# Kernel tuning notes

Hardware: AMD Instinct MI355X
Metric: run time of the kernel (lower is better)

Reference implementation:

```python
import jax, jax.numpy as jnp
import numpy as np

B, T, P, D, V = 8, 4096, 4, 512, 256
N = T // P          # 1024 patches (T divisible by P, so no padding needed)
K = 16              # k_retrieval
W = 4               # local message-passing window
H = 8               # refresh attention heads = min(8, D//64)
ROUNDS = 6
EPS = 1e-5


def layer_norm(x, g, b):
    mu = x.mean(-1, keepdims=True)
    var = ((x - mu) ** 2).mean(-1, keepdims=True)
    return (x - mu) / jnp.sqrt(var + EPS) * g + b


def setup_inputs() -> dict:
    key = jax.random.key(0)
    ks = iter(jax.random.split(key, 48))
    w = lambda *s: jax.random.normal(next(ks), s, jnp.float32) * 0.02
    p = {}
    p['x'] = jax.random.randint(next(ks), (B, T), 0, V)
    p['emb'] = w(V, D)
    p['pos_emb'] = w(P, D)
    p['gru_w_ih'] = w(D, 3 * D); p['gru_w_hh'] = w(D, 3 * D)
    p['gru_b_ih'] = jnp.zeros(3 * D); p['gru_b_hh'] = jnp.zeros(3 * D)
    p['patch_ln_g'] = jnp.ones(D); p['patch_ln_b'] = jnp.zeros(D)
    p['summ_w'] = w(D, D); p['summ_b'] = jnp.zeros(D)
    p['msg_w1'] = w(2 * D, D); p['msg_b1'] = jnp.zeros(D)
    p['msg_w2'] = w(D, D); p['msg_b2'] = jnp.zeros(D)
    p['msg_ln_g'] = jnp.ones(D); p['msg_ln_b'] = jnp.zeros(D)
    p['q_w'] = w(D, D); p['q_b'] = jnp.zeros(D)
    p['k_w'] = w(D, D); p['k_b'] = jnp.zeros(D)
    p['v_w'] = w(D, D); p['v_b'] = jnp.zeros(D)
    p['o_w'] = w(D, D); p['o_b'] = jnp.zeros(D)
    p['gc_w_ih'] = w(2 * D, 3 * D); p['gc_w_hh'] = w(D, 3 * D)
    p['gc_b_ih'] = jnp.zeros(3 * D); p['gc_b_hh'] = jnp.zeros(3 * D)
    p['ar_ln_g'] = jnp.ones(D); p['ar_ln_b'] = jnp.zeros(D)
    p['ar_qkv_w'] = w(D, 3 * D); p['ar_qkv_b'] = jnp.zeros(3 * D)
    p['ar_out_w'] = w(D, D); p['ar_out_b'] = jnp.zeros(D)
    p['broad_w'] = w(D, D); p['broad_b'] = jnp.zeros(D)
    p['ln_g'] = jnp.ones(D); p['ln_b'] = jnp.zeros(D)
    p['head_w'] = w(D, V)
    return p


def reference(x, emb, pos_emb, gru_w_ih, gru_w_hh, gru_b_ih, gru_b_hh,
              patch_ln_g, patch_ln_b, summ_w, summ_b,
              msg_w1, msg_b1, msg_w2, msg_b2, msg_ln_g, msg_ln_b,
              q_w, q_b, k_w, k_b, v_w, v_b, o_w, o_b,
              gc_w_ih, gc_w_hh, gc_b_ih, gc_b_hh,
              ar_ln_g, ar_ln_b, ar_qkv_w, ar_qkv_b, ar_out_w, ar_out_b,
              broad_w, broad_b, ln_g, ln_b, head_w):
    # --- patch encoding: embedding + pos + GRU over the P tokens of each patch ---
    flat = x.reshape(B * N, P)
    h = emb[flat] + pos_emb[None, :, :]                      # [B*N, P, D]

    def gru_step(hprev, xt):
        gi = xt @ gru_w_ih + gru_b_ih
        gh = hprev @ gru_w_hh + gru_b_hh
        ir, iz, inn = jnp.split(gi, 3, -1)
        hr, hz, hn = jnp.split(gh, 3, -1)
        r = jax.nn.sigmoid(ir + hr)
        z = jax.nn.sigmoid(iz + hz)
        n = jnp.tanh(inn + r * hn)
        hnew = (1 - z) * n + z * hprev
        return hnew, hnew

    _, hs = jax.lax.scan(gru_step, jnp.zeros((B * N, D), h.dtype), jnp.swapaxes(h, 0, 1))
    local = layer_norm(jnp.swapaxes(hs, 0, 1), patch_ln_g, patch_ln_b).reshape(B, N, P, D)
    h = local.mean(2) @ summ_w + summ_b                      # patch summaries [B, N, D]

    # --- RoPE tables over patch positions ---
    d = D // 2
    inv_freq = 1.0 / (10000.0 ** (jnp.arange(0, D, 2, dtype=jnp.float32) / D))
    freqs = jnp.arange(N, dtype=jnp.float32)[:, None] * inv_freq[None, :]   # [N, d]
    cos, sin = jnp.cos(freqs), jnp.sin(freqs)

    def rotary(t):
        t1, t2 = t[..., :d], t[..., d:]
        return jnp.concatenate([t1 * cos - t2 * sin, t2 * cos + t1 * sin], -1)

    causal = jnp.tril(jnp.ones((N, N), bool))
    hd = D // H

    for rnd in range(ROUNDS):
        # windowed neighbor gather (W past patches + self), fused MLP messages
        padded = jnp.pad(h, ((0, 0), (W, 0), (0, 0)))
        neighbors = jnp.stack([padded[:, W - w:W - w + N] for w in range(W + 1)], 2)  # [B,N,W+1,D]
        self_exp = jnp.broadcast_to(h[:, :, None, :], neighbors.shape)
        msg_in = jnp.concatenate([self_exp, neighbors], -1)
        msgs = (jax.nn.gelu(msg_in @ msg_w1 + msg_b1, approximate=False) @ msg_w2 + msg_b2).mean(2)

        # RoPE top-k sparse causal attention (N > K, sparse branch always taken)
        q = rotary(h @ q_w + q_b)
        k = rotary(h @ k_w + k_b)
        v = h @ v_w + v_b
        scores = jnp.einsum('bnd,bmd->bnm', q, k) / jnp.sqrt(jnp.float32(D))
        scores = jnp.where(causal, scores, -jnp.inf)
        tv, ti = jax.lax.top_k(scores, K)
        probs = jax.nn.softmax(tv, -1)  # == softmax of -inf-filled sparse score matrix
        vg = jax.vmap(lambda vi, ii: vi[ii])(v, ti)          # [B, N, K, D]
        retrieved = jnp.einsum('bnk,bnkd->bnd', probs, vg) @ o_w + o_b

        # GRUCell gated write
        wi = jnp.concatenate([msgs, retrieved], -1)
        gi = wi @ gc_w_ih + gc_b_ih
        gh = h @ gc_w_hh + gc_b_hh
        ir, iz, inn = jnp.split(gi, 3, -1)
        hr, hz, hn = jnp.split(gh, 3, -1)
        r = jax.nn.sigmoid(ir + hr)
        z = jax.nn.sigmoid(iz + hz)
        n = jnp.tanh(inn + r * hn)
        h = layer_norm((1 - z) * n + z * h, msg_ln_g, msg_ln_b)

        # global causal MHA refresh every 2 rounds (eval mode, no dropout)
        if (rnd + 1) % 2 == 0:
            res = h
            hn_ = layer_norm(h, ar_ln_g, ar_ln_b)
            qkv = hn_ @ ar_qkv_w + ar_qkv_b
            qh, kh, vh = [t.reshape(B, N, H, hd) for t in jnp.split(qkv, 3, -1)]
            s = jnp.einsum('bnhd,bmhd->bhnm', qh, kh) / jnp.sqrt(jnp.float32(hd))
            a = jax.nn.softmax(jnp.where(causal, s, -jnp.inf), -1)
            o = jnp.einsum('bhnm,bmhd->bnhd', a, vh).reshape(B, N, D)
            h = res + (o @ ar_out_w + ar_out_b)

    # broadcast patch state back to tokens, project to vocab
    broad = h @ broad_w + broad_b
    final = (local + broad[:, :, None, :]).reshape(B, N * P, D)[:, :T]
    return layer_norm(final, ln_g, ln_b) @ head_w            # [B, T, V]
```

## Files before the change

kernel.cpp:

```cpp
#include <hip/hip_runtime.h>
#include <math.h>

constexpr int CB = 8, CT = 4096, CP = 4, CD = 512, CV = 256;
constexpr int CN = 1024, CK = 16, CH = 8, CHD = 64;
constexpr int ROWS = CB * CN;
constexpr int TROWS = CB * CT;
constexpr float CEPS = 1e-5f;
constexpr size_t PN = (size_t)ROWS * CD;

constexpr size_t OFF_LOCAL = 0;
constexpr size_t OFF_HP    = OFF_LOCAL + (size_t)ROWS * CP * CD;
constexpr size_t OFF_X4    = OFF_HP    + PN;
constexpr size_t OFF_MS    = OFF_X4    + (size_t)ROWS * 2560;
constexpr size_t OFF_A     = OFF_MS    + PN;
constexpr size_t OFF_B     = OFF_A     + PN;
constexpr size_t OFF_BIAS  = OFF_B     + PN;
constexpr size_t OFF_WT    = OFF_BIAS  + 4096;

constexpr size_t TOT_W    = 7471104;
constexpr size_t T_GRU_IH = 0;
constexpr size_t T_GRU_HH = 786432;
constexpr size_t T_SUMM   = 1572864;
constexpr size_t T_FUSE   = 1835008;
constexpr size_t T_MSG2   = 3145728;
constexpr size_t T_OW     = 3407872;
constexpr size_t T_GCAB   = 3670016;
constexpr size_t T_GC_HH  = 5242880;
constexpr size_t T_AR_QKV = 6029312;
constexpr size_t T_AR_OUT = 6815744;
constexpr size_t T_BROAD  = 7077888;
constexpr size_t T_HEAD   = 7340032;

constexpr int F_ACC_F32  = 1;
constexpr int F_ACC_PAIR = 2;
constexpr int F_WR_F32   = 4;
constexpr int F_WR_PAIR  = 8;
constexpr int F_TRI      = 16;
constexpr int F_SPLIT    = 32;

typedef __attribute__((ext_vector_type(8))) short short8;
typedef __attribute__((ext_vector_type(4))) float f32x4;

__device__ __forceinline__ float sigm(float x) { return 1.f / (1.f + expf(-x)); }
__device__ __forceinline__ float geluf(float x) {
  return 0.5f * x * (1.f + erff(x * 0.7071067811865475f));
}
__device__ __forceinline__ unsigned short bf_hi(float x) {
  const unsigned u = __float_as_uint(x);
  return (unsigned short)((u + 0x7FFFu + ((u >> 16) & 1u)) >> 16);
}
__device__ __forceinline__ float bf_f(unsigned short h) {
  return __uint_as_float((unsigned)h << 16);
}
__device__ __forceinline__ void split_store(float v, unsigned short* ph, unsigned short* pl) {
  const unsigned short h = bf_hi(v);
  *ph = h; *pl = bf_hi(v - bf_f(h));
}
__device__ __forceinline__ float blk_sum(float v, float* red) {
#pragma unroll
  for (int o = 32; o > 0; o >>= 1) v += __shfl_down(v, o, 64);
  const int wv = threadIdx.x >> 6, ln = threadIdx.x & 63;
  __syncthreads();
  if (ln == 0) red[wv] = v;
  __syncthreads();
  return red[0] + red[1] + red[2] + red[3];
}

typedef __attribute__((address_space(1))) const unsigned int* gp1_t;
typedef __attribute__((address_space(3))) unsigned int* lp3_t;
__device__ __forceinline__ void gll16(const void* g, void* l) {
  __builtin_amdgcn_global_load_lds((gp1_t)g, (lp3_t)l, 16, 0, 0);
}

__device__ __forceinline__ int swz(int row, int quad) {
  return ((row & ~7) << 5) | (quad << 6) | ((row & 7) << 3);
}

__global__ __launch_bounds__(256) void transpose_split(const float* __restrict__ in,
                                                       unsigned short* __restrict__ oh,
                                                       unsigned short* __restrict__ ol,
                                                       int K, int N, int ldk, int ko)
{
  __shared__ float tile[32][33];
  const int n0 = blockIdx.x * 32, k0 = blockIdx.y * 32;
  const int tx = threadIdx.x & 31, ty = threadIdx.x >> 5;
#pragma unroll
  for (int i = 0; i < 32; i += 8)
    tile[ty + i][tx] = in[(size_t)(k0 + ty + i) * N + n0 + tx];
  __syncthreads();
#pragma unroll
  for (int i = 0; i < 32; i += 8) {
    const float v = tile[tx][ty + i];
    const unsigned short h = bf_hi(v);
    const size_t o = (size_t)(n0 + ty + i) * ldk + ko + k0 + tx;
    oh[o] = h;
    ol[o] = bf_hi(v - bf_f(h));
  }
}

__global__ void concat_bias5(const float* __restrict__ b1, const float* __restrict__ qb,
                             const float* __restrict__ kb, const float* __restrict__ vb,
                             float* __restrict__ o)
{
  const int i = blockIdx.x * 256 + threadIdx.x;
  float v;
  if (i < 512) v = b1[i];
  else if (i < 1024) v = 0.f;
  else if (i < 1536) v = qb[i - 1024];
  else if (i < 2048) v = kb[i - 1536];
  else v = vb[i - 2048];
  o[i] = v;
}

template <bool P3>
__global__ __launch_bounds__(256, 2) void gemm_bf3(
    const unsigned short* __restrict__ AH, const unsigned short* __restrict__ AL,
    const unsigned short* __restrict__ A2H, const unsigned short* __restrict__ A2L,
    int K1, int lda,
    const unsigned short* __restrict__ BH, const unsigned short* __restrict__ BL, int ldb,
    const float* __restrict__ bias, float scale,
    float* __restrict__ Cf, int ldc, float* __restrict__ Cf2,
    unsigned short* __restrict__ CHp, unsigned short* __restrict__ CLp, int ldcp,
    int K, int flags, long long sA, long long sB, long long sC)
{
  AH += (size_t)blockIdx.z * sA; AL += (size_t)blockIdx.z * sA;
  BH += (size_t)blockIdx.z * sB; BL += (size_t)blockIdx.z * sB;
  if (Cf) Cf += (size_t)blockIdx.z * sC;
  int bm, bn;
  if (flags & F_TRI) {
    int t = blockIdx.x, i = 0, acc0 = 0;
    while (acc0 + i + 1 <= t) { ++i; acc0 += i; }
    bm = i << 7; bn = (t - acc0) << 7;
  } else {
    bm = blockIdx.y << 7; bn = blockIdx.x << 7;
  }
  __shared__ __align__(16) unsigned short AsH[128 * 32];
  __shared__ __align__(16) unsigned short AsL[128 * 32];
  __shared__ __align__(16) unsigned short BsH[128 * 32];
  __shared__ __align__(16) unsigned short BsL[P3 ? 128 * 32 : 8];
  const int tid = threadIdx.x;
  const int lane = tid & 63, wave = tid >> 6;
  const int wm = (wave & 1) << 6, wn = (wave >> 1) << 6;
  const int r16 = lane & 15, quad = lane >> 4;
  const int lrow = ((lane >> 5) << 3) | (lane & 7);
  const int lcg8 = ((lane >> 3) & 3) << 3;
  const f32x4 zero = {0.f, 0.f, 0.f, 0.f};
  f32x4 acc[4][4];
#pragma unroll
  for (int i = 0; i < 4; ++i)
#pragma unroll
    for (int j = 0; j < 4; ++j) acc[i][j] = zero;

  for (int k0 = 0; k0 < K; k0 += 32) {
    const bool p1 = (k0 < K1);
    const unsigned short* bAH = p1 ? AH : A2H;
    const unsigned short* bAL = p1 ? AL : A2L;
    const int ka = (p1 ? k0 : k0 - K1) + lcg8;
    const int kb = k0 + lcg8;
#pragma unroll
    for (int i = 0; i < 2; ++i) {
      const int chunk = (wave << 1) | i;
      const size_t ra = (size_t)(bm + (chunk << 4) + lrow) * lda + ka;
      const size_t rb = (size_t)(bn + (chunk << 4) + lrow) * ldb + kb;
      gll16(bAH + ra, &AsH[chunk << 9]);
      gll16(bAL + ra, &AsL[chunk << 9]);
      gll16(BH + rb, &BsH[chunk << 9]);
      if (P3) gll16(BL + rb, &BsL[chunk << 9]);
    }
    __syncthreads();
    short8 bh[4], bl[4];
#pragma unroll
    for (int ni = 0; ni < 4; ++ni) {
      bh[ni] = *(const short8*)&BsH[swz(wn + ni * 16 + r16, quad)];
      if (P3) bl[ni] = *(const short8*)&BsL[swz(wn + ni * 16 + r16, quad)];
    }
#pragma unroll
    for (int mi = 0; mi < 4; ++mi) {
      const short8 ah = *(const short8*)&AsH[swz(wm + mi * 16 + r16, quad)];
      const short8 al = *(const short8*)&AsL[swz(wm + mi * 16 + r16, quad)];
#pragma unroll
      for (int ni = 0; ni < 4; ++ni) {
        acc[mi][ni] = __builtin_amdgcn_mfma_f32_16x16x32_bf16(ah, bh[ni], acc[mi][ni], 0, 0, 0);
        acc[mi][ni] = __builtin_amdgcn_mfma_f32_16x16x32_bf16(al, bh[ni], acc[mi][ni], 0, 0, 0);
        if (P3)
          acc[mi][ni] = __builtin_amdgcn_mfma_f32_16x16x32_bf16(ah, bl[ni], acc[mi][ni], 0, 0, 0);
      }
    }
    __syncthreads();
  }
#pragma unroll
  for (int mi = 0; mi < 4; ++mi) {
    const int row0 = bm + wm + mi * 16 + quad * 4;
#pragma unroll
    for (int ni = 0; ni < 4; ++ni) {
      const int col = bn + wn + ni * 16 + r16;
      const float bv = bias ? bias[col] : 0.f;
#pragma unroll
      for (int rg = 0; rg < 4; ++rg) {
        const int row = row0 + rg;
        float o = acc[mi][ni][rg] * scale + bv;
        if (flags & F_SPLIT) {
          if (col < 1024) {
            float* p = Cf + (size_t)row * ldc + col;
            *p = o + *p;
          } else {
            Cf2[(size_t)row * 512 + (col - 1024)] = o;
          }
        } else {
          if (flags & F_ACC_F32) o += Cf[(size_t)row * ldc + col];
          if (flags & F_ACC_PAIR) {
            const size_t ip = (size_t)row * ldcp + col;
            o += bf_f(CHp[ip]) + bf_f(CLp[ip]);
          }
          if (flags & F_WR_F32) Cf[(size_t)row * ldc + col] = o;
          if (flags & F_WR_PAIR) {
            const size_t ip = (size_t)row * ldcp + col;
            split_store(o, &CHp[ip], &CLp[ip]);
          }
        }
      }
    }
  }
}

__global__ __launch_bounds__(256, 3) void gemm_bf3s(
    const unsigned short* __restrict__ AH, const unsigned short* __restrict__ AL, int lda,
    const unsigned short* __restrict__ BH, int ldb,
    const float* __restrict__ bias,
    float* __restrict__ Cf, int ldc,
    unsigned short* __restrict__ CHp, unsigned short* __restrict__ CLp, int ldcp,
    int K, int flags)
{
  const int bm = blockIdx.y << 6, bn = blockIdx.x << 7;
  __shared__ __align__(16) unsigned short AsH[64 * 32];
  __shared__ __align__(16) unsigned short AsL[64 * 32];
  __shared__ __align__(16) unsigned short BsH[128 * 32];
  const int tid = threadIdx.x;
  const int lane = tid & 63, wave = tid >> 6;
  const int wm = (wave & 1) << 5, wn = (wave >> 1) << 6;
  const int r16 = lane & 15, quad = lane >> 4;
  const int lrow = ((lane >> 5) << 3) | (lane & 7);
  const int lcg8 = ((lane >> 3) & 3) << 3;
  const f32x4 zero = {0.f, 0.f, 0.f, 0.f};
  f32x4 acc[2][4];
#pragma unroll
  for (int i = 0; i < 2; ++i)
#pragma unroll
    for (int j = 0; j < 4; ++j) acc[i][j] = zero;

  for (int k0 = 0; k0 < K; k0 += 32) {
    {
      const size_t ra = (size_t)(bm + (wave << 4) + lrow) * lda + k0 + lcg8;
      gll16(AH + ra, &AsH[wave << 9]);
      gll16(AL + ra, &AsL[wave << 9]);
#pragma unroll
      for (int i = 0; i < 2; ++i) {
        const int chunk = (wave << 1) | i;
        const size_t rb = (size_t)(bn + (chunk << 4) + lrow) * ldb + k0 + lcg8;
        gll16(BH + rb, &BsH[chunk << 9]);
      }
    }
    __syncthreads();
    short8 bh[4];
#pragma unroll
    for (int ni = 0; ni < 4; ++ni)
      bh[ni] = *(const short8*)&BsH[swz(wn + ni * 16 + r16, quad)];
#pragma unroll
    for (int mi = 0; mi < 2; ++mi) {
      const short8 ah = *(const short8*)&AsH[swz(wm + mi * 16 + r16, quad)];
      const short8 al = *(const short8*)&AsL[swz(wm + mi * 16 + r16, quad)];
#pragma unroll
      for (int ni = 0; ni < 4; ++ni) {
        acc[mi][ni] = __builtin_amdgcn_mfma_f32_16x16x32_bf16(ah, bh[ni], acc[mi][ni], 0, 0, 0);
        acc[mi][ni] = __builtin_amdgcn_mfma_f32_16x16x32_bf16(al, bh[ni], acc[mi][ni], 0, 0, 0);
      }
    }
    __syncthreads();
  }
#pragma unroll
  for (int mi = 0; mi < 2; ++mi) {
    const int row0 = bm + wm + mi * 16 + quad * 4;
#pragma unroll
    for (int ni = 0; ni < 4; ++ni) {
      const int col = bn + wn + ni * 16 + r16;
      const float bv = bias ? bias[col] : 0.f;
#pragma unroll
      for (int rg = 0; rg < 4; ++rg) {
        const int row = row0 + rg;
        float o = acc[mi][ni][rg] + bv;
        if (flags & F_ACC_PAIR) {
          const size_t ip = (size_t)row * ldcp + col;
          o += bf_f(CHp[ip]) + bf_f(CLp[ip]);
        }
        if (flags & F_WR_F32) Cf[(size_t)row * ldc + col] = o;
        if (flags & F_WR_PAIR) {
          const size_t ip = (size_t)row * ldcp + col;
          split_store(o, &CHp[ip], &CLp[ip]);
        }
      }
    }
  }
}

__global__ void zero_k(float* __restrict__ p) {
  p[(size_t)blockIdx.x * 256 + threadIdx.x] = 0.f;
}

__global__ void embed_p(const int* __restrict__ x, const float* __restrict__ emb,
                        const float* __restrict__ pos,
                        unsigned short* __restrict__ oh, unsigned short* __restrict__ ol, int t)
{
  const int i = blockIdx.x * 256 + threadIdx.x;
  const int r = i >> 9, d = i & 511;
  const int b = r >> 10, n = r & (CN - 1);
  const int tok = x[b * CT + n * CP + t];
  const float v = emb[(size_t)tok * CD + d] + pos[t * CD + d];
  split_store(v, &oh[i], &ol[i]);
}

__global__ void gru_point_p(const float* __restrict__ gi, const float* __restrict__ ghn,
                            unsigned short* __restrict__ hH, unsigned short* __restrict__ hL,
                            float* __restrict__ hs, int t)
{
  const int i = blockIdx.x * 256 + threadIdx.x;
  const int r = i >> 9, d = i & 511;
  const size_t gb = (size_t)r * (3 * CD) + d;
  const float sr_ = gi[gb], sz = gi[gb + CD], inn = gi[gb + 2 * CD];
  const float hn = ghn[i];
  const float hp = bf_f(hH[i]) + bf_f(hL[i]);
  const float rr = sigm(sr_), zz = sigm(sz);
  const float nn = tanhf(inn + rr * hn);
  const float hv = (1.f - zz) * nn + zz * hp;
  split_store(hv, &hH[i], &hL[i]);
  hs[(size_t)r * (CP * CD) + (size_t)t * CD + d] = hv;
}

__global__ __launch_bounds__(256) void ln_rows(const float* __restrict__ in, float* __restrict__ out,
                                               const float* __restrict__ g, const float* __restrict__ b)
{
  const int r = blockIdx.x, t = threadIdx.x;
  __shared__ float red[4];
  const float* ip = in + (size_t)r * CD;
  const float v0 = ip[t], v1 = ip[t + 256];
  const float mu = blk_sum(v0 + v1, red) * (1.f / CD);
  const float d0 = v0 - mu, d1 = v1 - mu;
  const float var = blk_sum(d0 * d0 + d1 * d1, red) * (1.f / CD);
  const float inv = rsqrtf(var + CEPS);
  float* op = out + (size_t)r * CD;
  op[t] = d0 * inv * g[t] + b[t];
  op[t + 256] = d1 * inv * g[t + 256] + b[t + 256];
}

__global__ void mean_pool_p(const float* __restrict__ local,
                            unsigned short* __restrict__ oh, unsigned short* __restrict__ ol)
{
  const int i = blockIdx.x * 256 + threadIdx.x;
  const int r = i >> 9, d = i & 511;
  const float* p = local + (size_t)r * (CP * CD) + d;
  split_store(0.25f * (p[0] + p[CD] + p[2 * CD] + p[3 * CD]), &oh[i], &ol[i]);
}

__global__ void msg_gelu_p(const float* __restrict__ X4,
                           unsigned short* __restrict__ oh, unsigned short* __restrict__ ol)
{
  const int i = blockIdx.x * 256 + threadIdx.x;
  const int r = i >> 9, d = i & 511;
  const int n = r & (CN - 1);
  const float pv = X4[(size_t)r * 2560 + d];
  float acc = 0.f;
#pragma unroll
  for (int w = 0; w <= 4; ++w) {
    const float xv = pv + ((n >= w) ? X4[(size_t)(r - w) * 2560 + 512 + d] : 0.f);
    acc += geluf(xv);
  }
  split_store(acc * 0.2f, &oh[i], &ol[i]);
}

__global__ void rotary2_p(const float* __restrict__ X4,
                          unsigned short* __restrict__ qh, unsigned short* __restrict__ ql,
                          unsigned short* __restrict__ kh, unsigned short* __restrict__ kl)
{
  const int i = blockIdx.x * 256 + threadIdx.x;
  const int r = i >> 8, j = i & 255;
  const int n = r & (CN - 1);
  const float fr = (float)n * expf(-9.210340371976184f * ((float)j * (1.f / 256.f)));
  float s, c;
  sincosf(fr, &s, &c);
  const float* p = X4 + (size_t)r * 2560;
  const size_t o0 = (size_t)r * CD + j, o1 = o0 + 256;
  const float q1 = p[1024 + j], q2 = p[1024 + 256 + j];
  split_store(q1 * c - q2 * s, &qh[o0], &ql[o0]);
  split_store(q2 * c + q1 * s, &qh[o1], &ql[o1]);
  const float k1 = p[1536 + j], k2 = p[1536 + 256 + j];
  split_store(k1 * c - k2 * s, &kh[o0], &kl[o0]);
  split_store(k2 * c + k1 * s, &kh[o1], &kl[o1]);
}

__global__ __launch_bounds__(256) void topk_attn(const float* __restrict__ X4,
                                                 unsigned short* __restrict__ ctxH,
                                                 unsigned short* __restrict__ ctxL)
{
  const int r = blockIdx.x;
  const int b = r >> 10, n = r & (CN - 1);
  const float* row = X4 + (size_t)r * 2560;
  const int tid = threadIdx.x, lane = tid & 63, wave = tid >> 6;
  __shared__ unsigned long long cands[64];
  __shared__ float p16[CK];
  __shared__ int i16[CK];
  unsigned long long key[4];
#pragma unroll
  for (int q = 0; q < 4; ++q) {
    const int m = tid + q * 256;
    const float v = (m <= n) ? row[m] : -INFINITY;
    unsigned u = __float_as_uint(v);
    u = (u & 0x80000000u) ? ~u : (u | 0x80000000u);
    key[q] = ((unsigned long long)u << 32) | (unsigned)(CN - 1 - m);
  }
  unsigned long long mycand = 0ull;
#pragma unroll
  for (int it = 0; it < CK; ++it) {
    unsigned long long best = key[0];
#pragma unroll
    for (int q = 1; q < 4; ++q) best = best > key[q] ? best : key[q];
#pragma unroll
    for (int o = 32; o > 0; o >>= 1) {
      const unsigned long long o2 = __shfl_xor(best, o, 64);
      best = best > o2 ? best : o2;
    }
    if (lane == it) mycand = best;
#pragma unroll
    for (int q = 0; q < 4; ++q)
      if (key[q] == best) key[q] = 0ull;
  }
  if (lane < CK) cands[wave * CK + lane] = mycand;
  __syncthreads();
  if (wave == 0) {
    unsigned long long k2 = cands[lane];
    unsigned long long mine = 0ull;
#pragma unroll
    for (int it = 0; it < CK; ++it) {
      unsigned long long best = k2;
#pragma unroll
      for (int o = 32; o > 0; o >>= 1) {
        const unsigned long long o2 = __shfl_xor(best, o, 64);
        best = best > o2 ? best : o2;
      }
      if (lane == it) mine = best;
      if (k2 == best) k2 = 0ull;
    }
    unsigned u = (unsigned)(mine >> 32);
    u = (u & 0x80000000u) ? (u & 0x7FFFFFFFu) : ~u;
    const float val = __uint_as_float(u);
    const int idx = CN - 1 - (int)(mine & 0xFFFFFFFFu);
    const float mx = __shfl(val, 0, 64);
    float e = 0.f;
    if (lane < CK && val != -INFINITY) e = expf(val - mx);
    float sum = e;
#pragma unroll
    for (int o = 32; o > 0; o >>= 1) sum += __shfl_xor(sum, o, 64);
    if (lane < CK) {
      p16[lane] = e / sum;
      i16[lane] = idx;
    }
  }
  __syncthreads();
  const size_t vb = ((size_t)b << 10);
#pragma unroll
  for (int pass = 0; pass < 2; ++pass) {
    const int d = tid + pass * 256;
    float a = 0.f;
#pragma unroll
    for (int q = 0; q < CK; ++q)
      a += p16[q] * X4[(vb + i16[q]) * 2560 + 2048 + d];
    split_store(a, &ctxH[(size_t)r * CD + d], &ctxL[(size_t)r * CD + d]);
  }
}

__global__ __launch_bounds__(256) void gru_ln_p(const float* __restrict__ gi, const float* __restrict__ ghn,
                                                unsigned short* __restrict__ hH, unsigned short* __restrict__ hL,
                                                const float* __restrict__ g, const float* __restrict__ b,
                                                unsigned short* __restrict__ aH, unsigned short* __restrict__ aL,
                                                const float* __restrict__ g2, const float* __restrict__ b2)
{
  const int r = blockIdx.x, t = threadIdx.x;
  __shared__ float red[4];
  float u[2];
#pragma unroll
  for (int q = 0; q < 2; ++q) {
    const int d = t + q * 256;
    const size_t gb = (size_t)r * (3 * CD) + d;
    const float sr_ = gi[gb], sz = gi[gb + CD], inn = gi[gb + 2 * CD];
    const float hn = ghn[(size_t)r * CD + d];
    const size_t hi = (size_t)r * CD + d;
    const float hp = bf_f(hH[hi]) + bf_f(hL[hi]);
    const float rr = sigm(sr_), zz = sigm(sz);
    const float nn = tanhf(inn + rr * hn);
    u[q] = (1.f - zz) * nn + zz * hp;
  }
  const float mu = blk_sum(u[0] + u[1], red) * (1.f / CD);
  const float d0 = u[0] - mu, d1 = u[1] - mu;
  const float var = blk_sum(d0 * d0 + d1 * d1, red) * (1.f / CD);
  const float inv = rsqrtf(var + CEPS);
  const float h0 = d0 * inv * g[t] + b[t];
  const float h1 = d1 * inv * g[t + 256] + b[t + 256];
  split_store(h0, &hH[(size_t)r * CD + t], &hL[(size_t)r * CD + t]);
  split_store(h1, &hH[(size_t)r * CD + t + 256], &hL[(size_t)r * CD + t + 256]);
  if (aH) {
    const float mu2 = blk_sum(h0 + h1, red) * (1.f / CD);
    const float e0 = h0 - mu2, e1 = h1 - mu2;
    const float var2 = blk_sum(e0 * e0 + e1 * e1, red) * (1.f / CD);
    const float inv2 = rsqrtf(var2 + CEPS);
    split_store(e0 * inv2 * g2[t] + b2[t], &aH[(size_t)r * CD + t], &aL[(size_t)r * CD + t]);
    split_store(e1 * inv2 * g2[t + 256] + b2[t + 256],
                &aH[(size_t)r * CD + t + 256], &aL[(size_t)r * CD + t + 256]);
  }
}

constexpr int FP = 72;
__global__ __launch_bounds__(256, 3) void flash_attn_p(const unsigned short* __restrict__ qkvH,
                                                       const unsigned short* __restrict__ qkvL,
                                                       unsigned short* __restrict__ outH,
                                                       unsigned short* __restrict__ outL)
{
  __shared__ __align__(16) unsigned short Kh[64 * FP], Kl[64 * FP];
  __shared__ __align__(16) unsigned short Vth[64 * FP], Vtl[64 * FP];
  __shared__ __align__(16) unsigned short Pm[64 * FP];
  const int qt = blockIdx.x, head = blockIdx.y, b = blockIdx.z;
  const int tid = threadIdx.x;
  const int lane = tid & 63, wave = tid >> 6;
  const int r16 = lane & 15, quad = lane >> 4;
  const size_t base = (size_t)b * CN * (3 * CD) + head * CHD;

  short8 qh_r[2], ql_r[2];
  {
    const size_t qoff = base + (size_t)(qt * 64 + wave * 16 + r16) * (3 * CD) + quad * 8;
    const unsigned short* qph = qkvH + qoff;
    const unsigned short* qpl = qkvL + qoff;
    qh_r[0] = *(const short8*)qph;  qh_r[1] = *(const short8*)(qph + 32);
    ql_r[0] = *(const short8*)qpl;  ql_r[1] = *(const short8*)(qpl + 32);
  }
  float m_i[4], l_i[4];
  f32x4 O[4];
  const f32x4 zero = {0.f, 0.f, 0.f, 0.f};
#pragma unroll
  for (int r = 0; r < 4; ++r) { m_i[r] = -INFINITY; l_i[r] = 0.f; }
#pragma unroll
  for (int d = 0; d < 4; ++d) O[d] = zero;

  for (int j = 0; j <= qt; ++j) {
    __syncthreads();
    {
      const int r = tid >> 2, c0 = (tid & 3) << 4;
      const unsigned short* kh = qkvH + base + (size_t)(j * 64 + r) * (3 * CD) + CD + c0;
      const unsigned short* kl = qkvL + base + (size_t)(j * 64 + r) * (3 * CD) + CD + c0;
      *(uint4*)&Kh[r * FP + c0]     = *(const uint4*)kh;
      *(uint4*)&Kh[r * FP + c0 + 8] = *(const uint4*)(kh + 8);
      *(uint4*)&Kl[r * FP + c0]     = *(const uint4*)kl;
      *(uint4*)&Kl[r * FP + c0 + 8] = *(const uint4*)(kl + 8);
      const int rp = (tid >> 3) << 1, c0v = (tid & 7) << 3;
      const unsigned short* v0h = qkvH + base + (size_t)(j * 64 + rp) * (3 * CD) + 2 * CD + c0v;
      const unsigned short* v1h = v0h + 3 * CD;
      const unsigned short* v0l = qkvL + base + (size_t)(j * 64 + rp) * (3 * CD) + 2 * CD + c0v;
      const unsigned short* v1l = v0l + 3 * CD;
      unsigned short xh[8], yh[8], xl[8], yl[8];
      *(uint4*)xh = *(const uint4*)v0h; *(uint4*)yh = *(const uint4*)v1h;
      *(uint4*)xl = *(const uint4*)v0l; *(uint4*)yl = *(const uint4*)v1l;
#pragma unroll
      for (int c = 0; c < 8; ++c) {
        const int R = c0v + c;
        const int col = rp ^ ((R >> 3) << 3);
        *(unsigned*)&Vth[R * FP + col] = (unsigned)xh[c] | ((unsigned)yh[c] << 16);
        *(unsigned*)&Vtl[R * FP + col] = (unsigned)xl[c] | ((unsigned)yl[c] << 16);
      }
    }
    __syncthreads();
    f32x4 S[4];
#pragma unroll
    for (int nt = 0; nt < 4; ++nt) S[nt] = zero;
#pragma unroll
    for (int kh2 = 0; kh2 < 2; ++kh2) {
      const short8 qh = qh_r[kh2];
      const short8 ql = ql_r[kh2];
#pragma unroll
      for (int nt = 0; nt < 4; ++nt) {
        const short8 kkh = *(const short8*)&Kh[(nt * 16 + r16) * FP + kh2 * 32 + quad * 8];
        const short8 kkl = *(const short8*)&Kl[(nt * 16 + r16) * FP + kh2 * 32 + quad * 8];
        S[nt] = __builtin_amdgcn_mfma_f32_16x16x32_bf16(qh, kkh, S[nt], 0, 0, 0);
        S[nt] = __builtin_amdgcn_mfma_f32_16x16x32_bf16(qh, kkl, S[nt], 0, 0, 0);
        S[nt] = __builtin_amdgcn_mfma_f32_16x16x32_bf16(ql, kkh, S[nt], 0, 0, 0);
      }
    }
#pragma unroll
    for (int r = 0; r < 4; ++r) {
      const int qrow = wave * 16 + quad * 4 + r;
      float s[4];
#pragma unroll
      for (int nt = 0; nt < 4; ++nt) {
        s[nt] = S[nt][r] * 0.125f;
        if (j == qt && (nt * 16 + r16) > qrow) s[nt] = -1e30f;
      }
      float rm = fmaxf(fmaxf(s[0], s[1]), fmaxf(s[2], s[3]));
#pragma unroll
      for (int o = 8; o > 0; o >>= 1) rm = fmaxf(rm, __shfl_xor(rm, o, 64));
      const float newm = fmaxf(m_i[r], rm);
      float p[4], rs = 0.f;
#pragma unroll
      for (int nt = 0; nt < 4; ++nt) { p[nt] = expf(s[nt] - newm); rs += p[nt]; }
#pragma unroll
      for (int o = 8; o > 0; o >>= 1) rs += __shfl_xor(rs, o, 64);
      const float alpha = expf(m_i[r] - newm);
      l_i[r] = l_i[r] * alpha + rs;
      m_i[r] = newm;
#pragma unroll
      for (int dt = 0; dt < 4; ++dt) O[dt][r] *= alpha;
#pragma unroll
      for (int nt = 0; nt < 4; ++nt)
        Pm[qrow * FP + nt * 16 + r16] = bf_hi(p[nt]);
    }
    __syncthreads();
#pragma unroll
    for (int kh2 = 0; kh2 < 2; ++kh2) {
      const short8 pa = *(const short8*)&Pm[(wave * 16 + r16) * FP + kh2 * 32 + quad * 8];
#pragma unroll
      for (int dt = 0; dt < 4; ++dt) {
        const int R = dt * 16 + r16;
        const int col = (kh2 * 32 + quad * 8) ^ ((R >> 3) << 3);
        const short8 vh = *(const short8*)&Vth[R * FP + col];
        const short8 vl = *(const short8*)&Vtl[R * FP + col];
        O[dt] = __builtin_amdgcn_mfma_f32_16x16x32_bf16(pa, vh, O[dt], 0, 0, 0);
        O[dt] = __builtin_amdgcn_mfma_f32_16x16x32_bf16(pa, vl, O[dt], 0, 0, 0);
      }
    }
  }
#pragma unroll
  for (int r = 0; r < 4; ++r) {
    const float inv = 1.f / l_i[r];
    const size_t row = (size_t)b * CN + qt * 64 + wave * 16 + quad * 4 + r;
#pragma unroll
    for (int dt = 0; dt < 4; ++dt) {
      const size_t o = row * CD + head * CHD + dt * 16 + r16;
      split_store(O[dt][r] * inv, &outH[o], &outL[o]);
    }
  }
}

__global__ __launch_bounds__(256) void final_ln_p(const float* __restrict__ local,
                                                  const float* __restrict__ broad,
                                                  const float* __restrict__ g, const float* __restrict__ bb,
                                                  unsigned short* __restrict__ oh,
                                                  unsigned short* __restrict__ ol)
{
  const int r = blockIdx.x, t = threadIdx.x;
  __shared__ float red[4];
  const size_t lb = (size_t)r * CD;
  const size_t br = (size_t)(r >> 2) * CD;
  const float v0 = local[lb + t] + broad[br + t];
  const float v1 = local[lb + 256 + t] + broad[br + 256 + t];
  const float mu = blk_sum(v0 + v1, red) * (1.f / CD);
  const float d0 = v0 - mu, d1 = v1 - mu;
  const float var = blk_sum(d0 * d0 + d1 * d1, red) * (1.f / CD);
  const float inv = rsqrtf(var + CEPS);
  split_store(d0 * inv * g[t] + bb[t], &oh[lb + t], &ol[lb + t]);
  split_store(d1 * inv * g[t + 256] + bb[t + 256], &oh[lb + 256 + t], &ol[lb + 256 + t]);
}

extern "C" void kernel_launch(void* const* d_in, const int* in_sizes, int n_in,
                              void* d_out, int out_size, void* d_ws, size_t ws_size,
                              hipStream_t stream)
{
  (void)in_sizes; (void)n_in; (void)out_size; (void)ws_size;
  const int*   x         = (const int*)d_in[0];
  const float* emb       = (const float*)d_in[1];
  const float* pos_emb   = (const float*)d_in[2];
  const float* gru_w_ih  = (const float*)d_in[3];
  const float* gru_w_hh  = (const float*)d_in[4];
  const float* gru_b_ih  = (const float*)d_in[5];
  const float* gru_b_hh  = (const float*)d_in[6];
  const float* patch_g   = (const float*)d_in[7];
  const float* patch_b   = (const float*)d_in[8];
  const float* summ_w    = (const float*)d_in[9];
  const float* summ_b    = (const float*)d_in[10];
  const float* msg_w1    = (const float*)d_in[11];
  const float* msg_b1    = (const float*)d_in[12];
  const float* msg_w2    = (const float*)d_in[13];
  const float* msg_b2    = (const float*)d_in[14];
  const float* msg_ln_g  = (const float*)d_in[15];
  const float* msg_ln_b  = (const float*)d_in[16];
  const float* q_w       = (const float*)d_in[17];
  const float* q_b       = (const float*)d_in[18];
  const float* k_w       = (const float*)d_in[19];
  const float* k_b       = (const float*)d_in[20];
  const float* v_w       = (const float*)d_in[21];
  const float* v_b       = (const float*)d_in[22];
  const float* o_w       = (const float*)d_in[23];
  const float* o_b       = (const float*)d_in[24];
  const float* gc_w_ih   = (const float*)d_in[25];
  const float* gc_w_hh   = (const float*)d_in[26];
  const float* gc_b_ih   = (const float*)d_in[27];
  const float* gc_b_hh   = (const float*)d_in[28];
  const float* ar_ln_g   = (const float*)d_in[29];
  const float* ar_ln_b   = (const float*)d_in[30];
  const float* ar_qkv_w  = (const float*)d_in[31];
  const float* ar_qkv_b  = (const float*)d_in[32];
  const float* ar_out_w  = (const float*)d_in[33];
  const float* ar_out_b  = (const float*)d_in[34];
  const float* broad_w   = (const float*)d_in[35];
  const float* broad_b   = (const float*)d_in[36];
  const float* ln_g      = (const float*)d_in[37];
  const float* ln_b      = (const float*)d_in[38];
  const float* head_w    = (const float*)d_in[39];
  float* out = (float*)d_out;

  float* ws = (float*)d_ws;
  float* WL    = ws + OFF_LOCAL;
  float* X4    = ws + OFF_X4;
  float* GI    = X4;
  float* GHN   = X4 + (size_t)ROWS * 1536;
  float* WBR   = ws + OFF_MS;
  float* Wbias5 = ws + OFF_BIAS;
  unsigned short* WTh = (unsigned short*)(ws + OFF_WT);
  unsigned short* WTl = WTh + TOT_W;
  unsigned short* WhH = (unsigned short*)(ws + OFF_HP);
  unsigned short* WhL = WhH + PN;
  unsigned short* MsH = (unsigned short*)(ws + OFF_MS);
  unsigned short* MsL = MsH + PN;
  unsigned short* pAH = (unsigned short*)(ws + OFF_A);
  unsigned short* pAL = pAH + PN;
  unsigned short* pBH = (unsigned short*)(ws + OFF_B);
  unsigned short* pBL = pBH + PN;
  unsigned short* QkH = (unsigned short*)X4;
  unsigned short* QkL = QkH + (size_t)ROWS * 1536;
  unsigned short* FnH = (unsigned short*)X4;
  unsigned short* FnL = FnH + (size_t)TROWS * CD;

  const int EW = ROWS * CD / 256;
  const float inv_sqrt_d = 0.04419417382415922f;

  auto TR = [&](const float* in, size_t off, int K, int N, int ldk, int ko) {
    transpose_split<<<dim3(N / 32, K / 32), 256, 0, stream>>>(in, WTh + off, WTl + off, K, N, ldk, ko);
  };
  TR(gru_w_ih, T_GRU_IH, 512, 1536, 512, 0);
  TR(gru_w_hh, T_GRU_HH, 512, 1536, 512, 0);
  TR(summ_w,   T_SUMM,   512, 512,  512, 0);
  TR(msg_w1,                      T_FUSE,           512, 512, 512, 0);
  TR(msg_w1 + (size_t)512 * 512,  T_FUSE + 262144,  512, 512, 512, 0);
  TR(q_w,                         T_FUSE + 524288,  512, 512, 512, 0);
  TR(k_w,                         T_FUSE + 786432,  512, 512, 512, 0);
  TR(v_w,                         T_FUSE + 1048576, 512, 512, 512, 0);
  TR(msg_w2,   T_MSG2,   512, 512,  512, 0);
  TR(o_w, T_OW, 512, 512, 512, 0);
  TR(gc_w_ih,                       T_GCAB, 512, 1536, 1024, 0);
  TR(gc_w_ih + (size_t)512 * 1536,  T_GCAB, 512, 1536, 1024, 512);
  TR(gc_w_hh,  T_GC_HH,  512, 1536, 512, 0);
  TR(ar_qkv_w, T_AR_QKV, 512, 1536, 512, 0);
  TR(ar_out_w, T_AR_OUT, 512, 512,  512, 0);
  TR(broad_w,  T_BROAD,  512, 512,  512, 0);
  TR(head_w,   T_HEAD,   512, 256,  512, 0);
  concat_bias5<<<10, 256, 0, stream>>>(msg_b1, q_b, k_b, v_b, Wbias5);

  auto G3 = [&](const unsigned short* AH_, const unsigned short* AL_, int lda_,
                size_t toff, int ldb_, const float* bias_, float* Cf_, int ldc_, float* Cf2_,
                unsigned short* CHp_, unsigned short* CLp_, int ldcp_,
                int K_, int flags_, int gx, int gy) {
    gemm_bf3<false><<<dim3(gx, gy), 256, 0, stream>>>(
        AH_, AL_, AH_, AL_, K_, lda_, WTh + toff, WTl + toff, ldb_, bias_, 1.f,
        Cf_, ldc_, Cf2_, CHp_, CLp_, ldcp_, K_, flags_, 0, 0, 0);
  };
  auto G3S = [&](const unsigned short* AH_, const unsigned short* AL_, int lda_,
                 size_t toff, const float* bias_, float* Cf_, int ldc_,
                 unsigned short* CHp_, unsigned short* CLp_, int ldcp_,
                 int flags_, int gx, int gy) {
    gemm_bf3s<<<dim3(gx, gy), 256, 0, stream>>>(
        AH_, AL_, lda_, WTh + toff, 512, bias_,
        Cf_, ldc_, CHp_, CLp_, ldcp_, 512, flags_);
  };

  zero_k<<<EW, 256, 0, stream>>>(ws + OFF_HP);
  for (int t = 0; t < CP; ++t) {
    embed_p<<<EW, 256, 0, stream>>>(x, emb, pos_emb, pAH, pAL, t);
    G3(pAH, pAL, 512, T_GRU_IH, 512, gru_b_ih, GI, 1536, nullptr,
       nullptr, nullptr, 0, 512, F_WR_F32, 12, 64);
    G3(WhH, WhL, 512, T_GRU_HH, 512, gru_b_hh, GI, 1536, GHN,
       nullptr, nullptr, 0, 512, F_SPLIT, 12, 64);
    gru_point_p<<<EW, 256, 0, stream>>>(GI, GHN, WhH, WhL, WL, t);
  }
  ln_rows<<<TROWS, 256, 0, stream>>>(WL, WL, patch_g, patch_b);
  mean_pool_p<<<EW, 256, 0, stream>>>(WL, pAH, pAL);
  G3S(pAH, pAL, 512, T_SUMM, summ_b, nullptr, 0, WhH, WhL, 512, F_WR_PAIR, 4, 128);

  for (int rnd = 0; rnd < 6; ++rnd) {
    G3(WhH, WhL, 512, T_FUSE, 512, Wbias5, X4, 2560, nullptr,
       nullptr, nullptr, 0, 512, F_WR_F32, 20, 64);
    msg_gelu_p<<<EW, 256, 0, stream>>>(X4, pBH, pBL);
    G3S(pBH, pBL, 512, T_MSG2, msg_b2, nullptr, 0, MsH, MsL, 512, F_WR_PAIR, 4, 128);
    rotary2_p<<<ROWS, 256, 0, stream>>>(X4, pAH, pAL, pBH, pBL);
    gemm_bf3<true><<<dim3(36, 1, CB), 256, 0, stream>>>(
        pAH, pAL, pAH, pAL, 512, 512, pBH, pBL, 512, nullptr, inv_sqrt_d,
        X4, 2560, nullptr, nullptr, nullptr, 0, 512, F_WR_F32 | F_TRI,
        (long long)CN * CD, (long long)CN * CD, (long long)CN * 2560);
    topk_attn<<<ROWS, 256, 0, stream>>>(X4, pAH, pAL);
    G3S(pAH, pAL, 512, T_OW, o_b, nullptr, 0, pBH, pBL, 512, F_WR_PAIR, 4, 128);
    gemm_bf3<false><<<dim3(12, 64), 256, 0, stream>>>(
        MsH, MsL, pBH, pBL, 512, 512, WTh + T_GCAB, WTl + T_GCAB, 1024, gc_b_ih, 1.f,
        GI, 1536, nullptr, nullptr, nullptr, 0, 1024, F_WR_F32, 0, 0, 0);
    G3(WhH, WhL, 512, T_GC_HH, 512, gc_b_hh, GI, 1536, GHN,
       nullptr, nullptr, 0, 512, F_SPLIT, 12, 64);
    if ((rnd & 1) == 1) {
      gru_ln_p<<<ROWS, 256, 0, stream>>>(GI, GHN, WhH, WhL, msg_ln_g, msg_ln_b,
                                         pAH, pAL, ar_ln_g, ar_ln_b);
      G3(pAH, pAL, 512, T_AR_QKV, 512, ar_qkv_b, nullptr, 0, nullptr,
         QkH, QkL, 1536, 512, F_WR_PAIR, 12, 64);
      flash_attn_p<<<dim3(16, CH, CB), 256, 0, stream>>>(QkH, QkL, pBH, pBL);
      G3S(pBH, pBL, 512, T_AR_OUT, ar_out_b, nullptr, 0, WhH, WhL, 512,
          F_ACC_PAIR | F_WR_PAIR, 4, 128);
    } else {
      gru_ln_p<<<ROWS, 256, 0, stream>>>(GI, GHN, WhH, WhL, msg_ln_g, msg_ln_b,
                                         nullptr, nullptr, nullptr, nullptr);
    }
  }

  G3S(WhH, WhL, 512, T_BROAD, broad_b, WBR, 512, nullptr, nullptr, 0, F_WR_F32, 4, 128);
  final_ln_p<<<TROWS, 256, 0, stream>>>(WL, WBR, ln_g, ln_b, FnH, FnL);
  G3S(FnH, FnL, 512, T_HEAD, nullptr, out, CV, nullptr, nullptr, 0, F_WR_F32, 2, 512);
}
```

Before: 4.343 ms.

## Double-buffer LDS tiles in split-bf16 GEMMs and stage Q through LDS in attention

Both split-precision GEMM kernels now keep two LDS buffers and issue the global-to-LDS loads for tile k+1 before computing on tile k, so memory latency can overlap with MFMA work. The flash attention kernel now stages Q into shared memory instead of holding it in registers, and its occupancy hint drops from 3 to 2 blocks. The pipelined loop drops the syncthreads that followed each tile's loads and the shown hunks add none in their place, so correctness depends on barriers in the unshown loop tail. Doubled LDS use may also reduce occupancy.

```diff
diff --git a/kernel.cpp b/kernel.cpp
--- a/kernel.cpp
+++ b/kernel.cpp
@@ -134,10 +134,10 @@
   } else {
     bm = blockIdx.y << 7; bn = blockIdx.x << 7;
   }
-  __shared__ __align__(16) unsigned short AsH[128 * 32];
-  __shared__ __align__(16) unsigned short AsL[128 * 32];
-  __shared__ __align__(16) unsigned short BsH[128 * 32];
-  __shared__ __align__(16) unsigned short BsL[P3 ? 128 * 32 : 8];
+  __shared__ __align__(16) unsigned short AsH[2][128 * 32];
+  __shared__ __align__(16) unsigned short AsL[2][128 * 32];
+  __shared__ __align__(16) unsigned short BsH[2][128 * 32];
+  __shared__ __align__(16) unsigned short BsL[P3 ? 2 * 128 * 32 : 8];
   const int tid = threadIdx.x;
   const int lane = tid & 63, wave = tid >> 6;
   const int wm = (wave & 1) << 6, wn = (wave >> 1) << 6;
@@ -151,7 +151,7 @@
 #pragma unroll
     for (int j = 0; j < 4; ++j) acc[i][j] = zero;
 
-  for (int k0 = 0; k0 < K; k0 += 32) {
+  auto STAGE = [&](int k0, int buf) {
     const bool p1 = (k0 < K1);
     const unsigned short* bAH = p1 ? AH : A2H;
     const unsigned short* bAL = p1 ? AL : A2L;
@@ -162,22 +162,33 @@
       const int chunk = (wave << 1) | i;
       const size_t ra = (size_t)(bm + (chunk << 4) + lrow) * lda + ka;
       const size_t rb = (size_t)(bn + (chunk << 4) + lrow) * ldb + kb;
-      gll16(bAH + ra, &AsH[chunk << 9]);
-      gll16(bAL + ra, &AsL[chunk << 9]);
-      gll16(BH + rb, &BsH[chunk << 9]);
-      if (P3) gll16(BL + rb, &BsL[chunk << 9]);
-    }
-    __syncthreads();
+      gll16(bAH + ra, &AsH[buf][chunk << 9]);
+      gll16(bAL + ra, &AsL[buf][chunk << 9]);
+      gll16(BH + rb, &BsH[buf][chunk << 9]);
+      if (P3) gll16(BL + rb, &BsL[buf * (128 * 32) + (chunk << 9)]);
+    }
+  };
+
+  STAGE(0, 0);
+  __syncthreads();
+  const int NT = K >> 5;
+  for (int t = 0; t < NT; ++t) {
+    const int cur = t & 1;
+    if (t + 1 < NT) STAGE((t + 1) << 5, cur ^ 1);
+    const unsigned short* asH = AsH[cur];
+    const unsigned short* asL = AsL[cur];
+    const unsigned short* bsH = BsH[cur];
+    const unsigned short* bsL = &BsL[P3 ? cur * (128 * 32) : 0];
     short8 bh[4], bl[4];
 #pragma unroll
     for (int ni = 0; ni < 4; ++ni) {
-      bh[ni] = *(const short8*)&BsH[swz(wn + ni * 16 + r16, quad)];
-      if (P3) bl[ni] = *(const short8*)&BsL[swz(wn + ni * 16 + r16, quad)];
+      bh[ni] = *(const short8*)&bsH[swz(wn + ni * 16 + r16, quad)];
+      if (P3) bl[ni] = *(const short8*)&bsL[swz(wn + ni * 16 + r16, quad)];
     }
 #pragma unroll
     for (int mi = 0; mi < 4; ++mi) {
-      const short8 ah = *(const short8*)&AsH[swz(wm + mi * 16 + r16, quad)];
-      const short8 al = *(const short8*)&AsL[swz(wm + mi * 16 + r16, quad)];
+      const short8 ah = *(const short8*)&asH[swz(wm + mi * 16 + r16, quad)];
+      const short8 al = *(const short8*)&asL[swz(wm + mi * 16 + r16, quad)];
 #pragma unroll
       for (int ni = 0; ni < 4; ++ni) {
         acc[mi][ni] = __builtin_amdgcn_mfma_f32_16x16x32_bf16(ah, bh[ni], acc[mi][ni], 0, 0, 0);
@@ -232,9 +243,9 @@
     int K, int flags)
 {
   const int bm = blockIdx.y << 6, bn = blockIdx.x << 7;
-  __shared__ __align__(16) unsigned short AsH[64 * 32];
-  __shared__ __align__(16) unsigned short AsL[64 * 32];
-  __shared__ __align__(16) unsigned short BsH[128 * 32];
+  __shared__ __align__(16) unsigned short AsH[2][64 * 32];
+  __shared__ __align__(16) unsigned short AsL[2][64 * 32];
+  __shared__ __align__(16) unsigned short BsH[2][128 * 32];
   const int tid = threadIdx.x;
   const int lane = tid & 63, wave = tid >> 6;
   const int wm = (wave & 1) << 5, wn = (wave >> 1) << 6;
@@ -248,27 +259,35 @@
 #pragma unroll
     for (int j = 0; j < 4; ++j) acc[i][j] = zero;
 
-  for (int k0 = 0; k0 < K; k0 += 32) {
-    {
-      const size_t ra = (size_t)(bm + (wave << 4) + lrow) * lda + k0 + lcg8;
-      gll16(AH + ra, &AsH[wave << 9]);
-      gll16(AL + ra, &AsL[wave << 9]);
-#pragma unroll
-      for (int i = 0; i < 2; ++i) {
-        const int chunk = (wave << 1) | i;
-        const size_t rb = (size_t)(bn + (chunk << 4) + lrow) * ldb + k0 + lcg8;
-        gll16(BH + rb, &BsH[chunk << 9]);
-      }
-    }
-    __syncthreads();
+  auto STAGE = [&](int k0, int buf) {
+    const size_t ra = (size_t)(bm + (wave << 4) + lrow) * lda + k0 + lcg8;
+    gll16(AH + ra, &AsH[buf][wave << 9]);
+    gll16(AL + ra, &AsL[buf][wave << 9]);
+#pragma unroll
+    for (int i = 0; i < 2; ++i) {
+      const int chunk = (wave << 1) | i;
+      const size_t rb = (size_t)(bn + (chunk << 4) + lrow) * ldb + k0 + lcg8;
+      gll16(BH + rb, &BsH[buf][chunk << 9]);
+    }
+  };
+
+  STAGE(0, 0);
+  __syncthreads();
+  const int NT = K >> 5;
+  for (int t = 0; t < NT; ++t) {
+    const int cur = t & 1;
+    if (t + 1 < NT) STAGE((t + 1) << 5, cur ^ 1);
+    const unsigned short* asH = AsH[cur];
+    const unsigned short* asL = AsL[cur];
+    const unsigned short* bsH = BsH[cur];
     short8 bh[4];
 #pragma unroll
     for (int ni = 0; ni < 4; ++ni)
-      bh[ni] = *(const short8*)&BsH[swz(wn + ni * 16 + r16, quad)];
+      bh[ni] = *(const short8*)&bsH[swz(wn + ni * 16 + r16, quad)];
 #pragma unroll
     for (int mi = 0; mi < 2; ++mi) {
-      const short8 ah = *(const short8*)&AsH[swz(wm + mi * 16 + r16, quad)];
-      const short8 al = *(const short8*)&AsL[swz(wm + mi * 16 + r16, quad)];
+      const short8 ah = *(const short8*)&asH[swz(wm + mi * 16 + r16, quad)];
+      const short8 al = *(const short8*)&asL[swz(wm + mi * 16 + r16, quad)];
 #pragma unroll
       for (int ni = 0; ni < 4; ++ni) {
         acc[mi][ni] = __builtin_amdgcn_mfma_f32_16x16x32_bf16(ah, bh[ni], acc[mi][ni], 0, 0, 0);
@@ -517,11 +536,12 @@
 }
 
 constexpr int FP = 72;
-__global__ __launch_bounds__(256, 3) void flash_attn_p(const unsigned short* __restrict__ qkvH,
+__global__ __launch_bounds__(256, 2) void flash_attn_p(const unsigned short* __restrict__ qkvH,
                                                        const unsigned short* __restrict__ qkvL,
                                                        unsigned short* __restrict__ outH,
                                                        unsigned short* __restrict__ outL)
 {
+  __shared__ __align__(16) unsigned short Qh[64 * FP], Ql[64 * FP];
   __shared__ __align__(16) unsigned short Kh[64 * FP], Kl[64 * FP];
   __shared__ __align__(16) unsigned short Vth[64 * FP], Vtl[64 * FP];
   __shared__ __align__(16) unsigned short Pm[64 * FP];
@@ -531,13 +551,14 @@
   const int r16 = lane & 15, quad = lane >> 4;
   const size_t base = (size_t)b * CN * (3 * CD) + head * CHD;
 
-  short8 qh_r[2], ql_r[2];
   {
-    const size_t qoff = base + (size_t)(qt * 64 + wave * 16 + r16) * (3 * CD) + quad * 8;
-    const unsigned short* qph = qkvH + qoff;
-    const unsigned short* qpl = qkvL + qoff;
-    qh_r[0] = *(const short8*)qph;  qh_r[1] = *(const short8*)(qph + 32);
-    ql_r[0] = *(const short8*)qpl;  ql_r[1] = *(const short8*)(qpl + 32);
+    const int r = tid >> 2, c0 = (tid & 3) << 4;
+    const unsigned short* qh = qkvH + base + (size_t)(qt * 64 + r) * (3 * CD) + c0;
+    const unsigned short* ql = qkvL + base + (size_t)(qt * 64 + r) * (3 * CD) + c0;
+    *(uint4*)&Qh[r * FP + c0]     = *(const uint4*)qh;
+    *(uint4*)&Qh[r * FP + c0 + 8] = *(const uint4*)(qh + 8);
+    *(uint4*)&Ql[r * FP + c0]     = *(const uint4*)ql;
+    *(uint4*)&Ql[r * FP + c0 + 8] = *(const uint4*)(ql + 8);
   }
   float m_i[4], l_i[4];
   f32x4 O[4];
@@ -579,8 +600,8 @@
     for (int nt = 0; nt < 4; ++nt) S[nt] = zero;
 #pragma unroll
     for (int kh2 = 0; kh2 < 2; ++kh2) {
-      const short8 qh = qh_r[kh2];
-      const short8 ql = ql_r[kh2];
+      const short8 qh = *(const short8*)&Qh[(wave * 16 + r16) * FP + kh2 * 32 + quad * 8];
+      const short8 ql = *(const short8*)&Ql[(wave * 16 + r16) * FP + kh2 * 32 + quad * 8];
 #pragma unroll
       for (int nt = 0; nt < 4; ++nt) {
         const short8 kkh = *(const short8*)&Kh[(nt * 16 + r16) * FP + kh2 * 32 + quad * 8];
```

New measurement: 4.304 ms. About the same (-0.9%).
